# Optimization experiments

Measured on AMD Instinct MI355X. Metric: run time of the kernel, lower is better.

## Reference

```python
import jax, jax.numpy as jnp
import numpy as np

N_NODES = 50000
N_GRAPHS = 4
N_EDGES = 800000
D_IN = 128
D_OUT = 128


def setup_inputs() -> dict:
    key = jax.random.key(0)
    ks = jax.random.split(key, 7)
    x = jax.random.normal(ks[0], (N_NODES, D_IN), dtype=jnp.float32)
    edge_rows = jax.random.randint(ks[1], (N_GRAPHS, N_EDGES), 0, N_NODES, dtype=jnp.int32)
    edge_cols = jax.random.randint(ks[2], (N_GRAPHS, N_EDGES), 0, N_NODES, dtype=jnp.int32)
    edge_vals = jax.random.uniform(ks[3], (N_GRAPHS, N_EDGES), dtype=jnp.float32)
    W = jax.random.normal(ks[4], (N_GRAPHS, D_IN, D_OUT), dtype=jnp.float32) * (1.0 / np.sqrt(D_IN))
    mixing_weight = jax.random.uniform(ks[5], (N_GRAPHS, 1), dtype=jnp.float32, minval=-0.25, maxval=0.25)
    bias = jax.random.uniform(ks[6], (D_OUT,), dtype=jnp.float32, minval=-0.25, maxval=0.25)
    return {"x": x, "edge_rows": edge_rows, "edge_cols": edge_cols,
            "edge_vals": edge_vals, "W": W, "mixing_weight": mixing_weight, "bias": bias}


def _spmm(rows, cols, vals, dense):
    # sparse [N,N] (COO) @ dense [N,F] -> [N,F]
    gathered = dense[cols] * vals[:, None]          # [E, F]
    return jax.ops.segment_sum(gathered, rows, num_segments=N_NODES)


def reference(x, edge_rows, edge_cols, edge_vals, W, mixing_weight, bias):
    # Per-graph linear projection: [L, N, F_out]
    pre_sup = jnp.einsum('nd,ldf->lnf', x, W)
    # Per-graph spmm via vmap over graphs
    graph_outputs = jax.vmap(_spmm)(edge_rows, edge_cols, edge_vals, pre_sup)  # [L, N, F_out]
    # Weighted mix across graphs (tensordot + squeeze in torch)
    out = jnp.einsum('l,lnf->nf', mixing_weight[:, 0], graph_outputs)
    return out + bias
```

## Files before the change

kernel.cpp:

```cpp
#include <hip/hip_runtime.h>


constexpr int N = 50000;
constexpr int E = 800000;
constexpr int D = 128;
constexpr int L = 4;
constexpr int BSH = 4;
constexpr int NB = N >> BSH;
constexpr int NCHK = 100;
constexpr int CHUNK = E / NCHK;
constexpr int CAP = 1024;

typedef __attribute__((ext_vector_type(8))) short bf16x8;
typedef __attribute__((ext_vector_type(4))) float f32x4;
union U4B8 { uint4 u; bf16x8 b; };

__device__ inline unsigned bf16rne(unsigned u) {
    return (u + 0x7FFFu + ((u >> 16) & 1u)) >> 16;
}

__global__ __launch_bounds__(256) void cvt_x_kernel(
    const float* __restrict__ x, unsigned* __restrict__ xb)
{
    int i = blockIdx.x * 256 + threadIdx.x;
    int row = i >> 6, j = i & 63;
    int q = j >> 4, fl = j & 15;
    float2 v = *reinterpret_cast<const float2*>(x + (size_t)row * D + q * 32 + fl * 2);
    xb[((size_t)q * N + row) * 16 + fl] =
        bf16rne(__float_as_uint(v.x)) | (bf16rne(__float_as_uint(v.y)) << 16);
}

__global__ __launch_bounds__(256) void cvt_w_kernel(
    const float* __restrict__ W, const float* __restrict__ mix,
    unsigned* __restrict__ WbT)
{
    int idx = blockIdx.x * 256 + threadIdx.x;
    int f = idx & 127, dp = (idx >> 7) & 63, l = idx >> 13;
    float m = mix[l];
    float a = m * W[((size_t)l * D + 2 * dp) * D + f];
    float b = m * W[((size_t)l * D + 2 * dp + 1) * D + f];
    WbT[((size_t)l * D + f) * 64 + dp] =
        bf16rne(__float_as_uint(a)) | (bf16rne(__float_as_uint(b)) << 16);
}

__global__ __launch_bounds__(256) void hist_kernel(
    const int* __restrict__ edge_rows,
    unsigned short* __restrict__ pcnt,
    unsigned short* __restrict__ chunkoff)
{
    __shared__ int cnt[NB];
    __shared__ int psum[256];
    const int blk = blockIdx.x, g = blockIdx.y, tid = threadIdx.x;

    for (int i = tid; i < NB; i += 256) cnt[i] = 0;
    __syncthreads();

    const int* rows = edge_rows + (size_t)g * E + (size_t)blk * CHUNK;
    for (int i = tid; i < CHUNK; i += 256)
        atomicAdd(&cnt[rows[i] >> BSH], 1);
    __syncthreads();

    unsigned short* pc = pcnt + ((size_t)g * NCHK + blk) * NB;
    for (int i = tid; i < NB; i += 256) pc[i] = (unsigned short)cnt[i];
    __syncthreads();

    constexpr int CB = (NB + 255) / 256;
    const int base = tid * CB;
    int s = 0;
#pragma unroll
    for (int j = 0; j < CB; ++j) {
        int idx = base + j;
        if (idx < NB) s += cnt[idx];
    }
    psum[tid] = s;
    __syncthreads();
    for (int off = 1; off < 256; off <<= 1) {
        int v = (tid >= off) ? psum[tid - off] : 0;
        __syncthreads();
        psum[tid] += v;
        __syncthreads();
    }
    int carry = (tid == 0) ? 0 : psum[tid - 1];
#pragma unroll
    for (int j = 0; j < CB; ++j) {
        int idx = base + j;
        if (idx < NB) {
            int c = cnt[idx];
            cnt[idx] = carry;
            carry += c;
        }
    }
    __syncthreads();

    unsigned short* co = chunkoff + ((size_t)g * NCHK + blk) * NB;
    for (int i = tid; i < NB; i += 256) co[i] = (unsigned short)cnt[i];
}

__global__ __launch_bounds__(256) void scatter_kernel(
    const int* __restrict__ edge_rows,
    const int* __restrict__ edge_cols,
    const float* __restrict__ edge_vals,
    const unsigned short* __restrict__ chunkoff,
    unsigned* __restrict__ cvT,
    unsigned char* __restrict__ rlT)
{
    __shared__ unsigned cur[(NB + 1) / 2];
    __shared__ unsigned lcv[CHUNK];
    __shared__ unsigned char lrl[CHUNK];
    const int blk = blockIdx.x, g = blockIdx.y, tid = threadIdx.x;

    const unsigned short* co = chunkoff + ((size_t)g * NCHK + blk) * NB;
    for (int i = tid; i < (NB + 1) / 2; i += 256) {
        unsigned lo = co[2 * i];
        unsigned hi = (2 * i + 1 < NB) ? co[2 * i + 1] : 0u;
        cur[i] = lo | (hi << 16);
    }
    __syncthreads();

    const size_t eoff = (size_t)g * E + (size_t)blk * CHUNK;
    const int* rows = edge_rows + eoff;
    const int* cols = edge_cols + eoff;
    const float* vals = edge_vals + eoff;

    for (int i = tid; i < CHUNK; i += 256) {
        int r = rows[i];
        int b = r >> BSH;
        unsigned old = atomicAdd(&cur[b >> 1], (b & 1) ? 0x10000u : 1u);
        int pos = (old >> ((b & 1) * 16)) & 0xFFFFu;
        lcv[pos] = (unsigned)cols[i] | (bf16rne(__float_as_uint(vals[i])) << 16);
        lrl[pos] = (unsigned char)(r & 15);
    }
    __syncthreads();

    unsigned* cw = cvT + eoff;
    unsigned char* rw = rlT + eoff;
    for (int i = tid; i < CHUNK; i += 256) cw[i] = lcv[i];
    for (int i = tid * 4; i < CHUNK; i += 1024)
        *reinterpret_cast<uint*>(rw + i) = *reinterpret_cast<const uint*>(lrl + i);
}

__global__ __launch_bounds__(256) void scan1_kernel(
    unsigned short* __restrict__ pcnt, int* __restrict__ bstart)
{
    const int b = blockIdx.x * 256 + threadIdx.x;
    const int g = blockIdx.y;
    if (b >= NB) return;
    unsigned run = 0;
    unsigned short* p = pcnt + (size_t)g * NCHK * NB + b;
    for (int blk = 0; blk < NCHK; ++blk) {
        unsigned v = p[(size_t)blk * NB];
        p[(size_t)blk * NB] = (unsigned short)run;
        run += v;
    }
    bstart[(size_t)g * (NB + 1) + b] = (int)run;
}

__global__ __launch_bounds__(1024) void scan2_kernel(int* __restrict__ bstart)
{
    __shared__ int sums[1024];
    int* bs = bstart + (size_t)blockIdx.x * (NB + 1);
    const int t = threadIdx.x;
    int tv[4];
    int s = 0;
#pragma unroll
    for (int i = 0; i < 4; ++i) {
        int idx = t * 4 + i;
        tv[i] = (idx < NB) ? bs[idx] : 0;
        s += tv[i];
    }
    sums[t] = s;
    __syncthreads();
    for (int off = 1; off < 1024; off <<= 1) {
        int v = (t >= off) ? sums[t - off] : 0;
        __syncthreads();
        sums[t] += v;
        __syncthreads();
    }
    int ex = (t == 0) ? 0 : sums[t - 1];
#pragma unroll
    for (int i = 0; i < 4; ++i) {
        int idx = t * 4 + i;
        if (idx < NB) { bs[idx] = ex; ex += tv[i]; }
    }
    if (t == 0) bs[NB] = E;
}

__global__ __launch_bounds__(256) void sort2_kernel(
    const unsigned* __restrict__ cvT,
    const unsigned char* __restrict__ rlT,
    const unsigned short* __restrict__ pcnt,
    const unsigned short* __restrict__ chunkoff,
    const int* __restrict__ bstart,
    unsigned* __restrict__ cv,
    int* __restrict__ rowptr)
{
    __shared__ unsigned su_cv[CAP], ss_cv[CAP];
    __shared__ unsigned char su_rl[CAP];
    __shared__ int rc[17], rcur[16];
    const int b = blockIdx.x, g = blockIdx.y, tid = threadIdx.x;
    const int beg = bstart[(size_t)g * (NB + 1) + b];
    const int tot = bstart[(size_t)g * (NB + 1) + b + 1] - beg;
    const int cnt = tot < CAP ? tot : CAP;
    int* rp = rowptr + (size_t)g * (N + 1);
    if (b == 0 && tid == 0) rp[N] = E;
    if (tid < 17) rc[tid] = 0;

    if (tid < NCHK) {
        const int c = tid;
        const size_t pbase = ((size_t)g * NCHK + c) * NB + b;
        int off = pcnt[pbase];
        int nxt = (c == NCHK - 1) ? tot : (int)pcnt[pbase + NB];
        int len = nxt - off;
        const size_t wbase = (size_t)g * E + (size_t)c * CHUNK + chunkoff[pbase];
        const unsigned* cw = cvT + wbase;
        const unsigned char* rw = rlT + wbase;
        for (int i = 0; i < len; ++i) {
            int p = off + i;
            if (p < CAP) { su_cv[p] = cw[i]; su_rl[p] = rw[i]; }
        }
    }
    __syncthreads();

    for (int i = tid; i < cnt; i += 256) atomicAdd(&rc[su_rl[i] + 1], 1);
    __syncthreads();
    if (tid == 0) {
        int run = 0;
#pragma unroll
        for (int r = 1; r <= 16; ++r) { run += rc[r]; rc[r] = run; }
    }
    __syncthreads();
    if (tid < 16) {
        rcur[tid] = rc[tid];
        rp[b * 16 + tid] = beg + rc[tid];
    }
    __syncthreads();
    for (int i = tid; i < cnt; i += 256) {
        int p = atomicAdd(&rcur[su_rl[i]], 1);
        ss_cv[p] = su_cv[i];
    }
    __syncthreads();
    unsigned* cvg = cv + (size_t)g * E;
    for (int i = tid; i < cnt; i += 256) cvg[beg + i] = ss_cv[i];
}

__global__ __launch_bounds__(256) void fused_kernel(
    const unsigned* __restrict__ xb,
    const unsigned* __restrict__ cv,
    const int* __restrict__ rowptr,
    const unsigned* __restrict__ WbT,
    const float* __restrict__ bias,
    float* __restrict__ out,
    int q)
{
    __shared__ unsigned tile[16][16];

    const int tid = threadIdx.x;
    const int lane = tid & 63;
    const int wave = tid >> 6;
    const int sub = lane >> 4;
    const int fl = lane & 15;
    const int subbase = lane & 48;
    const int trow = wave * 4 + sub;
    const int row = blockIdx.x * 16 + trow;
    const int lrow = lane & 15, kgrp = lane >> 4;

    const unsigned* xq = xb + (size_t)q * N * 16;

    f32x4 acc[2] = {};

    for (int l = 0; l < L; ++l) {
        const unsigned* cvg = cv + (size_t)l * E;
        const int* rp = rowptr + (size_t)l * (N + 1);
        const int beg = rp[row], end = rp[row + 1];
        float accx = 0.f, accy = 0.f;

        for (int base = beg; base < end; base += 16) {
            const int cnt = end - base;
            unsigned cvr = (fl < cnt) ? cvg[base + fl] : 0u;
#pragma unroll
            for (int k = 0; k < 16; k += 4) {
                unsigned c0 = __shfl(cvr, subbase + k + 0);
                unsigned c1 = __shfl(cvr, subbase + k + 1);
                unsigned c2 = __shfl(cvr, subbase + k + 2);
                unsigned c3 = __shfl(cvr, subbase + k + 3);
                unsigned x0 = xq[(size_t)(c0 & 0xFFFFu) * 16 + fl];
                unsigned x1 = xq[(size_t)(c1 & 0xFFFFu) * 16 + fl];
                unsigned x2 = xq[(size_t)(c2 & 0xFFFFu) * 16 + fl];
                unsigned x3 = xq[(size_t)(c3 & 0xFFFFu) * 16 + fl];
                float v0 = __uint_as_float(c0 & 0xFFFF0000u);
                float v1 = __uint_as_float(c1 & 0xFFFF0000u);
                float v2 = __uint_as_float(c2 & 0xFFFF0000u);
                float v3 = __uint_as_float(c3 & 0xFFFF0000u);
                accx = fmaf(v0, __uint_as_float(x0 << 16), accx);
                accy = fmaf(v0, __uint_as_float(x0 & 0xFFFF0000u), accy);
                accx = fmaf(v1, __uint_as_float(x1 << 16), accx);
                accy = fmaf(v1, __uint_as_float(x1 & 0xFFFF0000u), accy);
                accx = fmaf(v2, __uint_as_float(x2 << 16), accx);
                accy = fmaf(v2, __uint_as_float(x2 & 0xFFFF0000u), accy);
                accx = fmaf(v3, __uint_as_float(x3 << 16), accx);
                accy = fmaf(v3, __uint_as_float(x3 & 0xFFFF0000u), accy);
            }
        }
        tile[trow][fl] = bf16rne(__float_as_uint(accx)) |
                         (bf16rne(__float_as_uint(accy)) << 16);
        __syncthreads();

        U4B8 a;
        a.u = *reinterpret_cast<const uint4*>(&tile[lrow][kgrp * 4]);
#pragma unroll
        for (int t = 0; t < 2; ++t) {
            const int f = wave * 32 + t * 16 + lrow;
            U4B8 bb;
            bb.u = *reinterpret_cast<const uint4*>(
                WbT + ((size_t)l * D + f) * 64 + q * 16 + kgrp * 4);
            acc[t] = __builtin_amdgcn_mfma_f32_16x16x32_bf16(a.b, bb.b, acc[t], 0, 0, 0);
        }
        __syncthreads();
    }

#pragma unroll
    for (int t = 0; t < 2; ++t) {
        const int f = wave * 32 + t * 16 + lrow;
#pragma unroll
        for (int i = 0; i < 4; ++i) {
            int orow = blockIdx.x * 16 + kgrp * 4 + i;
            float* p = out + (size_t)orow * D + f;
            float v = acc[t][i];
            *p = (q == 0) ? v + bias[f] : *p + v;
        }
    }
}

extern "C" void kernel_launch(void* const* d_in, const int* in_sizes, int n_in,
                              void* d_out, int out_size, void* d_ws, size_t ws_size,
                              hipStream_t stream)
{
    const float* x         = (const float*)d_in[0];
    const int*   edge_rows = (const int*)d_in[1];
    const int*   edge_cols = (const int*)d_in[2];
    const float* edge_vals = (const float*)d_in[3];
    const float* W         = (const float*)d_in[4];
    const float* mix       = (const float*)d_in[5];
    const float* bias      = (const float*)d_in[6];
    float* out = (float*)d_out;

    unsigned*       cvT      = (unsigned*)d_ws;
    unsigned char*  rlT      = (unsigned char*)(cvT + (size_t)L * E);
    unsigned short* pcnt     = (unsigned short*)(rlT + (size_t)L * E);
    unsigned short* chunkoff = pcnt + (size_t)L * NCHK * NB;
    int*            bstart   = (int*)(chunkoff + (size_t)L * NCHK * NB);
    int*            rowptr   = bstart + (size_t)L * (NB + 1);
    unsigned*       cv       = (unsigned*)(rowptr + (size_t)L * (N + 1));
    unsigned*       xb       = cv + (size_t)L * E;
    unsigned*       WbT      = xb + (size_t)4 * N * 16;

    cvt_x_kernel<<<(N * 64) / 256, 256, 0, stream>>>(x, xb);
    cvt_w_kernel<<<(L * D * 64) / 256, 256, 0, stream>>>(W, mix, WbT);
    hist_kernel<<<dim3(NCHK, L), 256, 0, stream>>>(edge_rows, pcnt, chunkoff);
    scatter_kernel<<<dim3(NCHK, L), 256, 0, stream>>>(edge_rows, edge_cols,
                                                      edge_vals, chunkoff, cvT, rlT);
    scan1_kernel<<<dim3((NB + 255) / 256, L), 256, 0, stream>>>(pcnt, bstart);
    scan2_kernel<<<L, 1024, 0, stream>>>(bstart);
    sort2_kernel<<<dim3(NB, L), 256, 0, stream>>>(cvT, rlT, pcnt, chunkoff, bstart,
                                                  cv, rowptr);

    for (int q = 0; q < 4; ++q)
        fused_kernel<<<N / 16, 256, 0, stream>>>(xb, cv, rowptr, WbT, bias, out, q);
}
```

Before: 303.9 us.

## Merge four feature-quarter launches into one kernel with LDS-staged edge lists

Replaces the four per-quarter fused launches with one kernel that loops over all feature quarters internally. Each block first stages its row-block edge lists for all graphs into shared memory, then reuses them for every quarter. Accumulators stay in registers, so the read-modify-write of the output between launches goes away. A double-buffered tile drops one barrier per iteration. The cost is a large LDS footprint (about 16KB for edges), which lowers occupancy, and rows with more than CAP edges per block are silently truncated.

```diff
diff --git a/kernel.cpp b/kernel.cpp
--- a/kernel.cpp
+++ b/kernel.cpp
@@ -243,17 +243,20 @@
     for (int i = tid; i < cnt; i += 256) cvg[beg + i] = ss_cv[i];
 }
 
-__global__ __launch_bounds__(256) void fused_kernel(
+__global__ __launch_bounds__(256) void fused_all_kernel(
     const unsigned* __restrict__ xb,
     const unsigned* __restrict__ cv,
     const int* __restrict__ rowptr,
+    const int* __restrict__ bstart,
     const unsigned* __restrict__ WbT,
     const float* __restrict__ bias,
-    float* __restrict__ out,
-    int q)
-{
-    __shared__ unsigned tile[16][16];
-
+    float* __restrict__ out)
+{
+    __shared__ unsigned scv[L][CAP];
+    __shared__ unsigned short rloc[L][17];
+    __shared__ unsigned tile[2][16][16];
+
+    const int b = blockIdx.x;
     const int tid = threadIdx.x;
     const int lane = tid & 63;
     const int wave = tid >> 6;
@@ -261,72 +264,83 @@
     const int fl = lane & 15;
     const int subbase = lane & 48;
     const int trow = wave * 4 + sub;
-    const int row = blockIdx.x * 16 + trow;
     const int lrow = lane & 15, kgrp = lane >> 4;
 
-    const unsigned* xq = xb + (size_t)q * N * 16;
+    for (int l = 0; l < L; ++l) {
+        const int beg = bstart[l * (NB + 1) + b];
+        int cnt = bstart[l * (NB + 1) + b + 1] - beg;
+        if (cnt > CAP) cnt = CAP;
+        const unsigned* src = cv + (size_t)l * E + beg;
+        for (int i = tid; i < cnt; i += 256) scv[l][i] = src[i];
+        if (tid < 17) {
+            int v = rowptr[l * (N + 1) + b * 16 + tid] - beg;
+            rloc[l][tid] = (unsigned short)(v > CAP ? CAP : v);
+        }
+    }
+    __syncthreads();
 
     f32x4 acc[2] = {};
-
-    for (int l = 0; l < L; ++l) {
-        const unsigned* cvg = cv + (size_t)l * E;
-        const int* rp = rowptr + (size_t)l * (N + 1);
-        const int beg = rp[row], end = rp[row + 1];
-        float accx = 0.f, accy = 0.f;
-
-        for (int base = beg; base < end; base += 16) {
-            const int cnt = end - base;
-            unsigned cvr = (fl < cnt) ? cvg[base + fl] : 0u;
-#pragma unroll
-            for (int k = 0; k < 16; k += 4) {
-                unsigned c0 = __shfl(cvr, subbase + k + 0);
-                unsigned c1 = __shfl(cvr, subbase + k + 1);
-                unsigned c2 = __shfl(cvr, subbase + k + 2);
-                unsigned c3 = __shfl(cvr, subbase + k + 3);
-                unsigned x0 = xq[(size_t)(c0 & 0xFFFFu) * 16 + fl];
-                unsigned x1 = xq[(size_t)(c1 & 0xFFFFu) * 16 + fl];
-                unsigned x2 = xq[(size_t)(c2 & 0xFFFFu) * 16 + fl];
-                unsigned x3 = xq[(size_t)(c3 & 0xFFFFu) * 16 + fl];
-                float v0 = __uint_as_float(c0 & 0xFFFF0000u);
-                float v1 = __uint_as_float(c1 & 0xFFFF0000u);
-                float v2 = __uint_as_float(c2 & 0xFFFF0000u);
-                float v3 = __uint_as_float(c3 & 0xFFFF0000u);
-                accx = fmaf(v0, __uint_as_float(x0 << 16), accx);
-                accy = fmaf(v0, __uint_as_float(x0 & 0xFFFF0000u), accy);
-                accx = fmaf(v1, __uint_as_float(x1 << 16), accx);
-                accy = fmaf(v1, __uint_as_float(x1 & 0xFFFF0000u), accy);
-                accx = fmaf(v2, __uint_as_float(x2 << 16), accx);
-                accy = fmaf(v2, __uint_as_float(x2 & 0xFFFF0000u), accy);
-                accx = fmaf(v3, __uint_as_float(x3 << 16), accx);
-                accy = fmaf(v3, __uint_as_float(x3 & 0xFFFF0000u), accy);
+    int tb = 0;
+
+    for (int q = 0; q < 4; ++q) {
+        const unsigned* xq = xb + (size_t)q * N * 16;
+        for (int l = 0; l < L; ++l) {
+            const int s0 = rloc[l][trow], s1 = rloc[l][trow + 1];
+            float accx = 0.f, accy = 0.f;
+            for (int base = s0; base < s1; base += 16) {
+                const int cnt = s1 - base;
+                unsigned cvr = (fl < cnt) ? scv[l][base + fl] : 0u;
+#pragma unroll
+                for (int k = 0; k < 16; k += 4) {
+                    unsigned c0 = __shfl(cvr, subbase + k + 0);
+                    unsigned c1 = __shfl(cvr, subbase + k + 1);
+                    unsigned c2 = __shfl(cvr, subbase + k + 2);
+                    unsigned c3 = __shfl(cvr, subbase + k + 3);
+                    unsigned x0 = xq[(size_t)(c0 & 0xFFFFu) * 16 + fl];
+                    unsigned x1 = xq[(size_t)(c1 & 0xFFFFu) * 16 + fl];
+                    unsigned x2 = xq[(size_t)(c2 & 0xFFFFu) * 16 + fl];
+                    unsigned x3 = xq[(size_t)(c3 & 0xFFFFu) * 16 + fl];
+                    float v0 = __uint_as_float(c0 & 0xFFFF0000u);
+                    float v1 = __uint_as_float(c1 & 0xFFFF0000u);
+                    float v2 = __uint_as_float(c2 & 0xFFFF0000u);
+                    float v3 = __uint_as_float(c3 & 0xFFFF0000u);
+                    accx = fmaf(v0, __uint_as_float(x0 << 16), accx);
+                    accy = fmaf(v0, __uint_as_float(x0 & 0xFFFF0000u), accy);
+                    accx = fmaf(v1, __uint_as_float(x1 << 16), accx);
+                    accy = fmaf(v1, __uint_as_float(x1 & 0xFFFF0000u), accy);
+                    accx = fmaf(v2, __uint_as_float(x2 << 16), accx);
+                    accy = fmaf(v2, __uint_as_float(x2 & 0xFFFF0000u), accy);
+                    accx = fmaf(v3, __uint_as_float(x3 << 16), accx);
+                    accy = fmaf(v3, __uint_as_float(x3 & 0xFFFF0000u), accy);
+                }
             }
-        }
-        tile[trow][fl] = bf16rne(__float_as_uint(accx)) |
-                         (bf16rne(__float_as_uint(accy)) << 16);
-        __syncthreads();
-
-        U4B8 a;
-        a.u = *reinterpret_cast<const uint4*>(&tile[lrow][kgrp * 4]);
-#pragma unroll
-        for (int t = 0; t < 2; ++t) {
-            const int f = wave * 32 + t * 16 + lrow;
-            U4B8 bb;
-            bb.u = *reinterpret_cast<const uint4*>(
-                WbT + ((size_t)l * D + f) * 64 + q * 16 + kgrp * 4);
-            acc[t] = __builtin_amdgcn_mfma_f32_16x16x32_bf16(a.b, bb.b, acc[t], 0, 0, 0);
-        }
-        __syncthreads();
+            tile[tb][trow][fl] = bf16rne(__float_as_uint(accx)) |
+                                 (bf16rne(__float_as_uint(accy)) << 16);
+            __syncthreads();
+
+            U4B8 a;
+            a.u = *reinterpret_cast<const uint4*>(&tile[tb][lrow][kgrp * 4]);
+#pragma unroll
+            for (int t = 0; t < 2; ++t) {
+                const int f = wave * 32 + t * 16 + lrow;
+                U4B8 bb;
+                bb.u = *reinterpret_cast<const uint4*>(
+                    WbT + ((size_t)l * D + f) * 64 + q * 16 + kgrp * 4);
+                acc[t] = __builtin_amdgcn_mfma_f32_16x16x32_bf16(
+                    a.b, bb.b, acc[t], 0, 0, 0);
+            }
+            tb ^= 1;
+        }
     }
 
 #pragma unroll
     for (int t = 0; t < 2; ++t) {
         const int f = wave * 32 + t * 16 + lrow;
+        const float bv = bias[f];
 #pragma unroll
         for (int i = 0; i < 4; ++i) {
-            int orow = blockIdx.x * 16 + kgrp * 4 + i;
-            float* p = out + (size_t)orow * D + f;
-            float v = acc[t][i];
-            *p = (q == 0) ? v + bias[f] : *p + v;
+            int orow = b * 16 + kgrp * 4 + i;
+            out[(size_t)orow * D + f] = acc[t][i] + bv;
         }
     }
 }
@@ -364,6 +378,6 @@
     sort2_kernel<<<dim3(NB, L), 256, 0, stream>>>(cvT, rlT, pcnt, chunkoff, bstart,
                                                   cv, rowptr);
 
-    for (int q = 0; q < 4; ++q)
-        fused_kernel<<<N / 16, 256, 0, stream>>>(xb, cv, rowptr, WbT, bias, out, q);
-}
+    fused_all_kernel<<<N / 16, 256, 0, stream>>>(xb, cv, rowptr, bstart,
+                                                 WbT, bias, out);
+}
```

Result: slower. 320.3 us (+5.4%).

## Process two 16-row blocks per workgroup with interleaved gathers and double-buffered tiles

Applied to the files above, without the earlier changes.

Each workgroup now handles two row blocks, interleaving the edge gathers of both rows in one loop to expose more independent memory loads per thread. The shared tile is double-buffered so the second barrier per graph iteration can be removed. This halves the grid size and raises register pressure. The joint loop runs to the longer of the two rows' edge counts, which may waste lanes.

```diff
diff --git a/kernel.cpp b/kernel.cpp
--- a/kernel.cpp
+++ b/kernel.cpp
@@ -252,7 +252,8 @@
     float* __restrict__ out,
     int q)
 {
-    __shared__ unsigned tile[16][16];
+    __shared__ unsigned tileA[2][16][16];
+    __shared__ unsigned tileB[2][16][16];
 
     const int tid = threadIdx.x;
     const int lane = tid & 63;
@@ -260,62 +261,98 @@
     const int sub = lane >> 4;
     const int fl = lane & 15;
     const int subbase = lane & 48;
-    const int trow = wave * 4 + sub;
-    const int row = blockIdx.x * 16 + trow;
+    const int srow = wave * 4 + sub;
+    const int b0 = blockIdx.x * 2;
+    const int b1 = b0 + 1;
+    const bool hasB1 = (b1 < NB);
+    const int rowA = b0 * 16 + srow;
+    const int rowB = hasB1 ? (b1 * 16 + srow) : rowA;
     const int lrow = lane & 15, kgrp = lane >> 4;
 
     const unsigned* xq = xb + (size_t)q * N * 16;
 
-    f32x4 acc[2] = {};
+    f32x4 acc[4] = {};
+    int tb = 0;
 
     for (int l = 0; l < L; ++l) {
         const unsigned* cvg = cv + (size_t)l * E;
         const int* rp = rowptr + (size_t)l * (N + 1);
-        const int beg = rp[row], end = rp[row + 1];
-        float accx = 0.f, accy = 0.f;
-
-        for (int base = beg; base < end; base += 16) {
-            const int cnt = end - base;
-            unsigned cvr = (fl < cnt) ? cvg[base + fl] : 0u;
+        int baseA = rp[rowA];
+        int nA = rp[rowA + 1] - baseA;
+        int baseB = rp[rowB];
+        int nB = rp[rowB + 1] - baseB;
+        if (!hasB1) nB = 0;
+        float axA = 0.f, ayA = 0.f, axB = 0.f, ayB = 0.f;
+
+        while (nA > 0 || nB > 0) {
+            unsigned cvrA = (fl < nA) ? cvg[baseA + fl] : 0u;
+            unsigned cvrB = (fl < nB) ? cvg[baseB + fl] : 0u;
 #pragma unroll
             for (int k = 0; k < 16; k += 4) {
-                unsigned c0 = __shfl(cvr, subbase + k + 0);
-                unsigned c1 = __shfl(cvr, subbase + k + 1);
-                unsigned c2 = __shfl(cvr, subbase + k + 2);
-                unsigned c3 = __shfl(cvr, subbase + k + 3);
-                unsigned x0 = xq[(size_t)(c0 & 0xFFFFu) * 16 + fl];
-                unsigned x1 = xq[(size_t)(c1 & 0xFFFFu) * 16 + fl];
-                unsigned x2 = xq[(size_t)(c2 & 0xFFFFu) * 16 + fl];
-                unsigned x3 = xq[(size_t)(c3 & 0xFFFFu) * 16 + fl];
-                float v0 = __uint_as_float(c0 & 0xFFFF0000u);
-                float v1 = __uint_as_float(c1 & 0xFFFF0000u);
-                float v2 = __uint_as_float(c2 & 0xFFFF0000u);
-                float v3 = __uint_as_float(c3 & 0xFFFF0000u);
-                accx = fmaf(v0, __uint_as_float(x0 << 16), accx);
-                accy = fmaf(v0, __uint_as_float(x0 & 0xFFFF0000u), accy);
-                accx = fmaf(v1, __uint_as_float(x1 << 16), accx);
-                accy = fmaf(v1, __uint_as_float(x1 & 0xFFFF0000u), accy);
-                accx = fmaf(v2, __uint_as_float(x2 << 16), accx);
-                accy = fmaf(v2, __uint_as_float(x2 & 0xFFFF0000u), accy);
-                accx = fmaf(v3, __uint_as_float(x3 << 16), accx);
-                accy = fmaf(v3, __uint_as_float(x3 & 0xFFFF0000u), accy);
+                const int kb = subbase + k;
+                unsigned a0 = __shfl(cvrA, kb + 0);
+                unsigned a1 = __shfl(cvrA, kb + 1);
+                unsigned a2 = __shfl(cvrA, kb + 2);
+                unsigned a3 = __shfl(cvrA, kb + 3);
+                unsigned b0v = __shfl(cvrB, kb + 0);
+                unsigned b1v = __shfl(cvrB, kb + 1);
+                unsigned b2v = __shfl(cvrB, kb + 2);
+                unsigned b3v = __shfl(cvrB, kb + 3);
+                unsigned xa0 = xq[(size_t)(a0 & 0xFFFFu) * 16 + fl];
+                unsigned xa1 = xq[(size_t)(a1 & 0xFFFFu) * 16 + fl];
+                unsigned xa2 = xq[(size_t)(a2 & 0xFFFFu) * 16 + fl];
+                unsigned xa3 = xq[(size_t)(a3 & 0xFFFFu) * 16 + fl];
+                unsigned xb0 = xq[(size_t)(b0v & 0xFFFFu) * 16 + fl];
+                unsigned xb1 = xq[(size_t)(b1v & 0xFFFFu) * 16 + fl];
+                unsigned xb2 = xq[(size_t)(b2v & 0xFFFFu) * 16 + fl];
+                unsigned xb3 = xq[(size_t)(b3v & 0xFFFFu) * 16 + fl];
+                float va0 = __uint_as_float(a0 & 0xFFFF0000u);
+                float va1 = __uint_as_float(a1 & 0xFFFF0000u);
+                float va2 = __uint_as_float(a2 & 0xFFFF0000u);
+                float va3 = __uint_as_float(a3 & 0xFFFF0000u);
+                float vb0 = __uint_as_float(b0v & 0xFFFF0000u);
+                float vb1 = __uint_as_float(b1v & 0xFFFF0000u);
+                float vb2 = __uint_as_float(b2v & 0xFFFF0000u);
+                float vb3 = __uint_as_float(b3v & 0xFFFF0000u);
+                axA = fmaf(va0, __uint_as_float(xa0 << 16), axA);
+                ayA = fmaf(va0, __uint_as_float(xa0 & 0xFFFF0000u), ayA);
+                axA = fmaf(va1, __uint_as_float(xa1 << 16), axA);
+                ayA = fmaf(va1, __uint_as_float(xa1 & 0xFFFF0000u), ayA);
+                axA = fmaf(va2, __uint_as_float(xa2 << 16), axA);
+                ayA = fmaf(va2, __uint_as_float(xa2 & 0xFFFF0000u), ayA);
+                axA = fmaf(va3, __uint_as_float(xa3 << 16), axA);
+                ayA = fmaf(va3, __uint_as_float(xa3 & 0xFFFF0000u), ayA);
+                axB = fmaf(vb0, __uint_as_float(xb0 << 16), axB);
+                ayB = fmaf(vb0, __uint_as_float(xb0 & 0xFFFF0000u), ayB);
+                axB = fmaf(vb1, __uint_as_float(xb1 << 16), axB);
+                ayB = fmaf(vb1, __uint_as_float(xb1 & 0xFFFF0000u), ayB);
+                axB = fmaf(vb2, __uint_as_float(xb2 << 16), axB);
+                ayB = fmaf(vb2, __uint_as_float(xb2 & 0xFFFF0000u), ayB);
+                axB = fmaf(vb3, __uint_as_float(xb3 << 16), axB);
+                ayB = fmaf(vb3, __uint_as_float(xb3 & 0xFFFF0000u), ayB);
             }
+            baseA += 16; nA -= 16;
+            baseB += 16; nB -= 16;
         }
-        tile[trow][fl] = bf16rne(__float_as_uint(accx)) |
-                         (bf16rne(__float_as_uint(accy)) << 16);
+        tileA[tb][srow][fl] = bf16rne(__float_as_uint(axA)) |
+                              (bf16rne(__float_as_uint(ayA)) << 16);
+        tileB[tb][srow][fl] = bf16rne(__float_as_uint(axB)) |
+                              (bf16rne(__float_as_uint(ayB)) << 16);
         __syncthreads();
 
-        U4B8 a;
-        a.u = *reinterpret_cast<const uint4*>(&tile[lrow][kgrp * 4]);
+        U4B8 aA, aB;
+        aA.u = *reinterpret_cast<const uint4*>(&tileA[tb][lrow][kgrp * 4]);
+        aB.u = *reinterpret_cast<const uint4*>(&tileB[tb][lrow][kgrp * 4]);
 #pragma unroll
         for (int t = 0; t < 2; ++t) {
             const int f = wave * 32 + t * 16 + lrow;
             U4B8 bb;
             bb.u = *reinterpret_cast<const uint4*>(
                 WbT + ((size_t)l * D + f) * 64 + q * 16 + kgrp * 4);
-            acc[t] = __builtin_amdgcn_mfma_f32_16x16x32_bf16(a.b, bb.b, acc[t], 0, 0, 0);
+            acc[t]     = __builtin_amdgcn_mfma_f32_16x16x32_bf16(aA.b, bb.b, acc[t], 0, 0, 0);
+            acc[2 + t] = __builtin_amdgcn_mfma_f32_16x16x32_bf16(aB.b, bb.b, acc[2 + t], 0, 0, 0);
         }
-        __syncthreads();
+        tb ^= 1;
     }
 
 #pragma unroll
@@ -323,10 +360,16 @@
         const int f = wave * 32 + t * 16 + lrow;
 #pragma unroll
         for (int i = 0; i < 4; ++i) {
-            int orow = blockIdx.x * 16 + kgrp * 4 + i;
-            float* p = out + (size_t)orow * D + f;
-            float v = acc[t][i];
-            *p = (q == 0) ? v + bias[f] : *p + v;
+            int orowA = b0 * 16 + kgrp * 4 + i;
+            float* pA = out + (size_t)orowA * D + f;
+            float vA = acc[t][i];
+            *pA = (q == 0) ? vA + bias[f] : *pA + vA;
+            if (hasB1) {
+                int orowB = b1 * 16 + kgrp * 4 + i;
+                float* pB = out + (size_t)orowB * D + f;
+                float vB = acc[2 + t][i];
+                *pB = (q == 0) ? vB + bias[f] : *pB + vB;
+            }
         }
     }
 }
@@ -365,5 +408,6 @@
                                                   cv, rowptr);
 
     for (int q = 0; q < 4; ++q)
-        fused_kernel<<<N / 16, 256, 0, stream>>>(xb, cv, rowptr, WbT, bias, out, q);
-}
+        fused_kernel<<<(NB + 1) / 2, 256, 0, stream>>>(xb, cv, rowptr, WbT,
+                                                       bias, out, q);
+}
```

Result: slower. 320.8 us (+5.6%).
